# Kernel optimization log

Hardware: AMD Instinct MI355X
Metric: run time of the kernel (lower is better)

Reference implementation:

```python
import jax, jax.numpy as jnp
import numpy as np

B, L, D = 4, 8192, 512


def setup_inputs() -> dict:
    key = jax.random.key(0)
    kx, kwg, kwc = jax.random.split(key, 3)
    x = jax.random.normal(kx, (B, L, D), dtype=jnp.float32)
    # Xavier-uniform init for DxD linears
    bound = float(np.sqrt(6.0 / (D + D)))
    Wg = jax.random.uniform(kwg, (D, D), minval=-bound, maxval=bound, dtype=jnp.float32)
    bg = jnp.ones((D,), dtype=jnp.float32)   # gate bias init to 1.0
    Wc = jax.random.uniform(kwc, (D, D), minval=-bound, maxval=bound, dtype=jnp.float32)
    bc = jnp.zeros((D,), dtype=jnp.float32)
    return {"x": x, "Wg": Wg, "bg": bg, "Wc": Wc, "bc": bc}


def _mingru_scan(gates, cands):
    # h_t = (1 - g_t) * h_{t-1} + g_t * c_t, h_0 = 0
    # linear recurrence h_t = a_t h_{t-1} + b_t with a = 1-g, b = g*c
    a = 1.0 - gates
    b = gates * cands

    def combine(left, right):
        a_l, b_l = left
        a_r, b_r = right
        return a_r * a_l, a_r * b_l + b_r

    _, h = jax.lax.associative_scan(combine, (a, b), axis=1)
    return h


def reference(x, Wg, bg, Wc, bc):
    gates = jax.nn.sigmoid(jnp.einsum('bld,ed->ble', x, Wg) + bg)
    cands = jnp.tanh(jnp.einsum('bld,ed->ble', x, Wc) + bc)
    return _mingru_scan(gates, cands)
```

## Files before the change

### kernel.cpp

```cpp
#include <hip/hip_runtime.h>
#include <stdint.h>
#include <stddef.h>

#define B_ 4
#define L_ 8192
#define D_ 512
#define M_ (B_*L_)
#define K_ 512
#define CHUNK 64
#define NC (L_/CHUNK)

typedef _Float16 f16;
typedef f16 f16x2 __attribute__((ext_vector_type(2)));
typedef f16 f16x4 __attribute__((ext_vector_type(4)));
typedef f16 f16x8 __attribute__((ext_vector_type(8)));
typedef __fp16 h16x2 __attribute__((ext_vector_type(2)));
typedef float f32x4 __attribute__((ext_vector_type(4)));

__device__ __forceinline__ uint32_t pack2(float a, float b) {
  h16x2 p = __builtin_amdgcn_cvt_pkrtz(a, b);
  return __builtin_bit_cast(uint32_t, p);
}

__device__ __forceinline__ void async16(const void* g, void* l) {
  __builtin_amdgcn_global_load_lds(
      (const __attribute__((address_space(1))) uint32_t*)g,
      (__attribute__((address_space(3))) uint32_t*)l,
      16, 0, 0);
}

__global__ __launch_bounds__(256) void cvt_x(const float* __restrict__ x,
                                             f16* __restrict__ xh) {
  int idx = (blockIdx.x * 256 + threadIdx.x) * 4;
  float4 v = *(const float4*)(x + idx);
  f16x4 o = {(f16)v.x, (f16)v.y, (f16)v.z, (f16)v.w};
  *(f16x4*)(xh + idx) = o;
}

__global__ __launch_bounds__(256) void pack_w(const float* __restrict__ Wg,
                                              const float* __restrict__ Wc,
                                              f16* __restrict__ wp) {
  int idx = (blockIdx.x * 256 + threadIdx.x) * 4;
  const float* src = (idx < 262144) ? (Wg + idx) : (Wc + (idx - 262144));
  float4 v = *(const float4*)src;
  f16x4 o = {(f16)v.x, (f16)v.y, (f16)v.z, (f16)v.w};
  *(f16x4*)(wp + idx) = o;
}

__global__ __launch_bounds__(256, 2) void gemm_act(
    const f16* __restrict__ Xh, const f16* __restrict__ Wp,
    const float* __restrict__ bg, const float* __restrict__ bc,
    uint32_t* __restrict__ AC) {
  __shared__ __align__(16) f16 sA[128 * 32];
  __shared__ __align__(16) f16 sBg[128 * 32];
  __shared__ __align__(16) f16 sBc[128 * 32];

  const int tid = threadIdx.x;
  const int id = blockIdx.x;
  const int xcd = id & 7;
  const int slot = id >> 3;
  const int g_ = xcd * 128 + slot;
  const int bm = g_ >> 2;
  const int bn = g_ & 3;

  const int lane = tid & 63;
  const int w = tid >> 6;
  const int wm = w >> 1, wn = w & 1;
  const int l15 = lane & 15, quad = lane >> 4;

  const int srow = tid >> 2;
  const int spc8 = (tid & 3) * 8;
  const f16* gA  = Xh + (size_t)(bm * 128 + srow) * K_ + spc8;
  const f16* gBg = Wp + (size_t)(bn * 128 + srow) * K_ + spc8;
  const f16* gBc = Wp + (size_t)(512 + bn * 128 + srow) * K_ + spc8;
  f16* lA  = sA  + tid * 8;
  f16* lBg = sBg + tid * 8;
  f16* lBc = sBc + tid * 8;

  f32x4 accG[4][4] = {};
  f32x4 accC[4][4] = {};

  for (int k0 = 0; k0 < K_; k0 += 32) {
    async16(gA + k0,  lA);
    async16(gA + (size_t)64 * K_ + k0,  lA  + 64 * 32);
    async16(gBg + k0, lBg);
    async16(gBg + (size_t)64 * K_ + k0, lBg + 64 * 32);
    async16(gBc + k0, lBc);
    async16(gBc + (size_t)64 * K_ + k0, lBc + 64 * 32);
    __syncthreads();

    f16x8 af[4], bgf[4], bcf[4];
#pragma unroll
    for (int i = 0; i < 4; i++)
      af[i]  = *(const f16x8*)(sA  + (wm * 64 + i * 16 + l15) * 32 + quad * 8);
#pragma unroll
    for (int j = 0; j < 4; j++) {
      bgf[j] = *(const f16x8*)(sBg + (wn * 64 + j * 16 + l15) * 32 + quad * 8);
      bcf[j] = *(const f16x8*)(sBc + (wn * 64 + j * 16 + l15) * 32 + quad * 8);
    }
#pragma unroll
    for (int i = 0; i < 4; i++)
#pragma unroll
      for (int j = 0; j < 4; j++) {
        accG[i][j] = __builtin_amdgcn_mfma_f32_16x16x32_f16(af[i], bgf[j], accG[i][j], 0, 0, 0);
        accC[i][j] = __builtin_amdgcn_mfma_f32_16x16x32_f16(af[i], bcf[j], accC[i][j], 0, 0, 0);
      }
    __syncthreads();
  }

#pragma unroll
  for (int j = 0; j < 4; j++) {
    const int col = bn * 128 + wn * 64 + j * 16 + l15;
    const float bgv = bg[col];
    const float bcv = bc[col];
#pragma unroll
    for (int i = 0; i < 4; i++) {
      const int mrow = bm * 128 + wm * 64 + i * 16 + quad * 4;
#pragma unroll
      for (int r = 0; r < 4; r++) {
        float yg = accG[i][j][r] + bgv;
        float yc = accC[i][j][r] + bcv;
        AC[(size_t)(mrow + r) * 512 + col] = pack2(yg, yc);
      }
    }
  }
}

__global__ __launch_bounds__(512) void scan_local(
    uint32_t* __restrict__ AC,
    float* __restrict__ cA, float* __restrict__ cB) {
  const int blk = blockIdx.x;
  const int d = threadIdx.x;
  const size_t base = (size_t)blk * CHUNK * 512 + d;
  float P = 1.0f, Q = 0.0f;
#pragma unroll 4
  for (int t = 0; t < CHUNK; t++) {
    const size_t i = base + (size_t)t * 512;
    f16x2 v = __builtin_bit_cast(f16x2, AC[i]);
    float yg = (float)v[0];
    float yc = (float)v[1];
    float a = 1.0f / (1.0f + __expf(yg));
    float e = __expf(fmaxf(-2.0f * yc, -30.0f));
    float c = (1.0f - e) / (1.0f + e);
    float b = (1.0f - a) * c;
    AC[i] = pack2(a, b);
    Q = fmaf(a, Q, b);
    P *= a;
  }
  cA[blk * 512 + d] = P;
  cB[blk * 512 + d] = Q;
}

__global__ __launch_bounds__(64) void scan_chunks(
    const float* __restrict__ cA, const float* __restrict__ cB,
    float* __restrict__ Hp) {
  const int b = blockIdx.x >> 3;
  const int d = ((blockIdx.x & 7) << 6) + threadIdx.x;
  float h = 0.0f;
#pragma unroll 8
  for (int ch = 0; ch < NC; ch++) {
    const int idx = (b * NC + ch) * 512 + d;
    Hp[idx] = h;
    h = fmaf(cA[idx], h, cB[idx]);
  }
}

__global__ __launch_bounds__(512) void scan_apply(
    const uint32_t* __restrict__ AC, const float* __restrict__ Hp,
    float* __restrict__ out) {
  const int blk = blockIdx.x;
  const int d = threadIdx.x;
  const size_t base = (size_t)blk * CHUNK * 512 + d;
  float h = Hp[blk * 512 + d];
#pragma unroll 4
  for (int t = 0; t < CHUNK; t++) {
    const size_t i = base + (size_t)t * 512;
    f16x2 v = __builtin_bit_cast(f16x2, AC[i]);
    h = fmaf((float)v[0], h, (float)v[1]);
    out[i] = h;
  }
}

extern "C" void kernel_launch(void* const* d_in, const int* in_sizes, int n_in,
                              void* d_out, int out_size, void* d_ws, size_t ws_size,
                              hipStream_t stream) {
  const float* x  = (const float*)d_in[0];
  const float* Wg = (const float*)d_in[1];
  const float* bg = (const float*)d_in[2];
  const float* Wc = (const float*)d_in[3];
  const float* bc = (const float*)d_in[4];
  float* out = (float*)d_out;

  char* ws = (char*)d_ws;
  f16*      xh = (f16*)(ws);
  f16*      wp = (f16*)(ws + 33554432);
  uint32_t* AC = (uint32_t*)(ws + 34603008);
  float*    cA = (float*)(ws + 101711872);
  float*    cB = (float*)(ws + 102760448);
  float*    Hp = (float*)(ws + 103809024);

  cvt_x<<<M_ * D_ / (256 * 4), 256, 0, stream>>>(x, xh);
  pack_w<<<2 * D_ * D_ / (256 * 4), 256, 0, stream>>>(Wg, Wc, wp);
  gemm_act<<<(M_ / 128) * 4, 256, 0, stream>>>(xh, wp, bg, bc, AC);
  scan_local<<<B_ * NC, 512, 0, stream>>>(AC, cA, cB);
  scan_chunks<<<32, 64, 0, stream>>>(cA, cB, Hp);
  scan_apply<<<B_ * NC, 512, 0, stream>>>(AC, Hp, out);
}
```

Measured before the change: 220.9 us.

## Fuse three-pass scan into single-pass decoupled look-back scan kernel

Replaces the scan_local, scan_chunks and scan_apply kernels with one kernel. It uses dynamic chunk IDs from an atomic counter and decoupled look-back over per-chunk flags. Each block keeps its transformed (a,b) pairs in registers, so they are never written back to global memory and re-read, and two launches disappear. It also merges the x and W conversion kernels into one prep kernel that resets the flags, and raises the GEMM occupancy hint to 4 blocks. In exchange, chunk carries are stored as packed fp16, which may cost precision, and spinning on flags adds serial latency across chunks.

```diff
diff --git a/kernel.cpp b/kernel.cpp
--- a/kernel.cpp
+++ b/kernel.cpp
@@ -8,7 +8,8 @@
 #define M_ (B_*L_)
 #define K_ 512
 #define CHUNK 64
-#define NC (L_/CHUNK)
+#define NCHUNK (M_/CHUNK)
+#define NC_SEQ (L_/CHUNK)
 
 typedef _Float16 f16;
 typedef f16 f16x2 __attribute__((ext_vector_type(2)));
@@ -29,25 +30,32 @@
       16, 0, 0);
 }
 
-__global__ __launch_bounds__(256) void cvt_x(const float* __restrict__ x,
-                                             f16* __restrict__ xh) {
-  int idx = (blockIdx.x * 256 + threadIdx.x) * 4;
-  float4 v = *(const float4*)(x + idx);
-  f16x4 o = {(f16)v.x, (f16)v.y, (f16)v.z, (f16)v.w};
-  *(f16x4*)(xh + idx) = o;
-}
-
-__global__ __launch_bounds__(256) void pack_w(const float* __restrict__ Wg,
-                                              const float* __restrict__ Wc,
-                                              f16* __restrict__ wp) {
-  int idx = (blockIdx.x * 256 + threadIdx.x) * 4;
-  const float* src = (idx < 262144) ? (Wg + idx) : (Wc + (idx - 262144));
-  float4 v = *(const float4*)src;
-  f16x4 o = {(f16)v.x, (f16)v.y, (f16)v.z, (f16)v.w};
-  *(f16x4*)(wp + idx) = o;
-}
-
-__global__ __launch_bounds__(256, 2) void gemm_act(
+__global__ __launch_bounds__(256) void prep(
+    const float* __restrict__ x, const float* __restrict__ Wg,
+    const float* __restrict__ Wc, f16* __restrict__ xh,
+    f16* __restrict__ wp, uint32_t* __restrict__ flags,
+    uint32_t* __restrict__ counter) {
+  const int blk = blockIdx.x;
+  const int tid = threadIdx.x;
+  if (blk < 16384) {
+    int idx = (blk * 256 + tid) * 4;
+    float4 v = *(const float4*)(x + idx);
+    f16x4 o = {(f16)v.x, (f16)v.y, (f16)v.z, (f16)v.w};
+    *(f16x4*)(xh + idx) = o;
+  } else if (blk < 16896) {
+    int idx = ((blk - 16384) * 256 + tid) * 4;
+    const float* src = (idx < 262144) ? (Wg + idx) : (Wc + (idx - 262144));
+    float4 v = *(const float4*)src;
+    f16x4 o = {(f16)v.x, (f16)v.y, (f16)v.z, (f16)v.w};
+    *(f16x4*)(wp + idx) = o;
+  } else {
+    flags[tid] = 0u;
+    flags[tid + 256] = 0u;
+    if (tid == 0) *counter = 0u;
+  }
+}
+
+__global__ __launch_bounds__(256, 4) void gemm_act(
     const f16* __restrict__ Xh, const f16* __restrict__ Wp,
     const float* __restrict__ bg, const float* __restrict__ bc,
     uint32_t* __restrict__ AC) {
@@ -126,58 +134,100 @@
   }
 }
 
-__global__ __launch_bounds__(512) void scan_local(
-    uint32_t* __restrict__ AC,
-    float* __restrict__ cA, float* __restrict__ cB) {
-  const int blk = blockIdx.x;
-  const int d = threadIdx.x;
-  const size_t base = (size_t)blk * CHUNK * 512 + d;
+__global__ __launch_bounds__(512, 4) void scan_lb(
+    const uint32_t* __restrict__ AC,
+    uint32_t* __restrict__ agg, uint32_t* __restrict__ inc,
+    volatile uint32_t* __restrict__ flags, uint32_t* __restrict__ counter,
+    float* __restrict__ out) {
+  __shared__ uint32_t s_vbid;
+  __shared__ uint32_t s_flag;
+  const int tid = threadIdx.x;
+  if (tid == 0) s_vbid = atomicAdd(counter, 1u) & (NCHUNK - 1);
+  __syncthreads();
+  const int v = (int)s_vbid;
+  const int ch = v & (NC_SEQ - 1);
+  const size_t base = (size_t)v * CHUNK * 512 + tid;
+
+  uint32_t ab[CHUNK];
   float P = 1.0f, Q = 0.0f;
-#pragma unroll 4
+#pragma unroll
   for (int t = 0; t < CHUNK; t++) {
-    const size_t i = base + (size_t)t * 512;
-    f16x2 v = __builtin_bit_cast(f16x2, AC[i]);
-    float yg = (float)v[0];
-    float yc = (float)v[1];
+    f16x2 pv = __builtin_bit_cast(f16x2, AC[base + (size_t)t * 512]);
+    float yg = (float)pv[0];
+    float yc = (float)pv[1];
     float a = 1.0f / (1.0f + __expf(yg));
     float e = __expf(fmaxf(-2.0f * yc, -30.0f));
     float c = (1.0f - e) / (1.0f + e);
     float b = (1.0f - a) * c;
-    AC[i] = pack2(a, b);
+    ab[t] = pack2(a, b);
     Q = fmaf(a, Q, b);
     P *= a;
   }
-  cA[blk * 512 + d] = P;
-  cB[blk * 512 + d] = Q;
-}
-
-__global__ __launch_bounds__(64) void scan_chunks(
-    const float* __restrict__ cA, const float* __restrict__ cB,
-    float* __restrict__ Hp) {
-  const int b = blockIdx.x >> 3;
-  const int d = ((blockIdx.x & 7) << 6) + threadIdx.x;
-  float h = 0.0f;
-#pragma unroll 8
-  for (int ch = 0; ch < NC; ch++) {
-    const int idx = (b * NC + ch) * 512 + d;
-    Hp[idx] = h;
-    h = fmaf(cA[idx], h, cB[idx]);
-  }
-}
-
-__global__ __launch_bounds__(512) void scan_apply(
-    const uint32_t* __restrict__ AC, const float* __restrict__ Hp,
-    float* __restrict__ out) {
-  const int blk = blockIdx.x;
-  const int d = threadIdx.x;
-  const size_t base = (size_t)blk * CHUNK * 512 + d;
-  float h = Hp[blk * 512 + d];
-#pragma unroll 4
+
+  uint32_t pq = pack2(P, Q);
+  float hpre;
+  if (ch == 0) {
+    __hip_atomic_store(&inc[v * 512 + tid], pq, __ATOMIC_RELAXED,
+                       __HIP_MEMORY_SCOPE_AGENT);
+    __threadfence();
+    __syncthreads();
+    if (tid == 0)
+      __hip_atomic_store((uint32_t*)&flags[v], 2u, __ATOMIC_RELEASE,
+                         __HIP_MEMORY_SCOPE_AGENT);
+    hpre = 0.0f;
+  } else {
+    __hip_atomic_store(&agg[v * 512 + tid], pq, __ATOMIC_RELAXED,
+                       __HIP_MEMORY_SCOPE_AGENT);
+    __threadfence();
+    __syncthreads();
+    if (tid == 0)
+      __hip_atomic_store((uint32_t*)&flags[v], 1u, __ATOMIC_RELEASE,
+                         __HIP_MEMORY_SCOPE_AGENT);
+
+    float Pr = 1.0f, Qr = 0.0f;
+    int j = v - 1;
+    for (;;) {
+      if (tid == 0) {
+        uint32_t f;
+        do {
+          f = __hip_atomic_load((uint32_t*)&flags[j], __ATOMIC_ACQUIRE,
+                                __HIP_MEMORY_SCOPE_AGENT);
+          if (f == 0) __builtin_amdgcn_s_sleep(8);
+        } while (f == 0);
+        s_flag = f;
+      }
+      __syncthreads();
+      const uint32_t f = s_flag;
+      const uint32_t* src = (f == 2) ? &inc[j * 512 + tid] : &agg[j * 512 + tid];
+      uint32_t pj = __hip_atomic_load(src, __ATOMIC_RELAXED,
+                                      __HIP_MEMORY_SCOPE_AGENT);
+      f16x2 vj = __builtin_bit_cast(f16x2, pj);
+      float Pj = (float)vj[0], Qj = (float)vj[1];
+      float Pr_old = Pr;
+      Pr = Pr * Pj;
+      Qr = fmaf(Pr_old, Qj, Qr);
+      __syncthreads();
+      if (f == 2) break;
+      j--;
+    }
+    float Pinc = P * Pr;
+    float Qinc = fmaf(P, Qr, Q);
+    __hip_atomic_store(&inc[v * 512 + tid], pack2(Pinc, Qinc),
+                       __ATOMIC_RELAXED, __HIP_MEMORY_SCOPE_AGENT);
+    __threadfence();
+    __syncthreads();
+    if (tid == 0)
+      __hip_atomic_store((uint32_t*)&flags[v], 2u, __ATOMIC_RELEASE,
+                         __HIP_MEMORY_SCOPE_AGENT);
+    hpre = Qr;
+  }
+
+  float h = hpre;
+#pragma unroll
   for (int t = 0; t < CHUNK; t++) {
-    const size_t i = base + (size_t)t * 512;
-    f16x2 v = __builtin_bit_cast(f16x2, AC[i]);
-    h = fmaf((float)v[0], h, (float)v[1]);
-    out[i] = h;
+    f16x2 vv = __builtin_bit_cast(f16x2, ab[t]);
+    h = fmaf((float)vv[0], h, (float)vv[1]);
+    out[base + (size_t)t * 512] = h;
   }
 }
 
@@ -192,17 +242,16 @@
   float* out = (float*)d_out;
 
   char* ws = (char*)d_ws;
-  f16*      xh = (f16*)(ws);
-  f16*      wp = (f16*)(ws + 33554432);
-  uint32_t* AC = (uint32_t*)(ws + 34603008);
-  float*    cA = (float*)(ws + 101711872);
-  float*    cB = (float*)(ws + 102760448);
-  float*    Hp = (float*)(ws + 103809024);
-
-  cvt_x<<<M_ * D_ / (256 * 4), 256, 0, stream>>>(x, xh);
-  pack_w<<<2 * D_ * D_ / (256 * 4), 256, 0, stream>>>(Wg, Wc, wp);
+  f16*      xh    = (f16*)(ws);
+  f16*      wp    = (f16*)(ws + 33554432);
+  uint32_t* AC    = (uint32_t*)(ws + 34603008);
+  uint32_t* agg   = (uint32_t*)(ws + 101711872);
+  uint32_t* inc   = (uint32_t*)(ws + 102760448);
+  uint32_t* flags = (uint32_t*)(ws + 103809024);
+  uint32_t* cnt   = (uint32_t*)(ws + 103811072);
+
+  prep<<<16897, 256, 0, stream>>>(x, Wg, Wc, xh, wp, flags, cnt);
   gemm_act<<<(M_ / 128) * 4, 256, 0, stream>>>(xh, wp, bg, bc, AC);
-  scan_local<<<B_ * NC, 512, 0, stream>>>(AC, cA, cB);
-  scan_chunks<<<32, 64, 0, stream>>>(cA, cB, Hp);
-  scan_apply<<<B_ * NC, 512, 0, stream>>>(AC, Hp, out);
-}
+
+  scan_lb<<<NCHUNK, 512, 0, stream>>>(AC, agg, inc, flags, cnt, out);
+}
```

Measured after the change: 820.4 us. 3.71x slower.
